# Kernel tuning notes

Measured on AMD Instinct MI355X. Metric: run time of the kernel, lower is better.

The kernel has to match this reference:

```python
import jax, jax.numpy as jnp
import numpy as np

N_STATE = 64
N_LAYERS = 4
D_MODEL = 512
D_OUT = 256
BATCH = 16
SEQLEN = 2048


def setup_inputs() -> dict:
    key = jax.random.key(0)
    ks = jax.random.split(key, 16)
    H, N, nl = D_MODEL, N_STATE, N_LAYERS
    inp = {}
    inp["x"] = jax.random.normal(ks[0], (BATCH, SEQLEN, D_MODEL), dtype=jnp.float32)
    # encoder / decoder dense
    inp["enc_w"] = jax.random.normal(ks[1], (D_MODEL, D_MODEL), jnp.float32) / np.sqrt(D_MODEL)
    inp["enc_b"] = jnp.zeros((D_MODEL,), jnp.float32)
    inp["dec_w"] = jax.random.normal(ks[2], (D_MODEL, D_OUT), jnp.float32) / np.sqrt(D_MODEL)
    inp["dec_b"] = jnp.zeros((D_OUT,), jnp.float32)
    # per-layer LayerNorm
    inp["ln_scale"] = jnp.ones((nl, D_MODEL), jnp.float32)
    inp["ln_bias"] = jnp.zeros((nl, D_MODEL), jnp.float32)
    # per-layer S4 DPLR params (stored as real/imag float pairs)
    inp["lambda_re"] = -0.5 * jnp.ones((nl, H, N), jnp.float32)
    inp["lambda_im"] = jnp.broadcast_to(np.pi * jnp.arange(N, dtype=jnp.float32), (nl, H, N))
    inp["p_re"] = jax.random.normal(ks[3], (nl, H, N), jnp.float32) * 0.5
    inp["p_im"] = jax.random.normal(ks[4], (nl, H, N), jnp.float32) * 0.5
    inp["b_re"] = jax.random.normal(ks[5], (nl, H, N), jnp.float32) * 0.5
    inp["b_im"] = jax.random.normal(ks[6], (nl, H, N), jnp.float32) * 0.5
    inp["c_re"] = jax.random.normal(ks[7], (nl, H, N), jnp.float32) * 0.5
    inp["c_im"] = jax.random.normal(ks[8], (nl, H, N), jnp.float32) * 0.5
    inp["log_step"] = jax.random.uniform(ks[9], (nl, H), jnp.float32, minval=np.log(1e-3), maxval=np.log(1e-1))
    inp["d_param"] = jnp.ones((nl, H), jnp.float32)
    # per-layer output Dense
    inp["out_w"] = jax.random.normal(ks[10], (nl, D_MODEL, D_MODEL), jnp.float32) / np.sqrt(D_MODEL)
    inp["out_b"] = jnp.zeros((nl, D_MODEL), jnp.float32)
    return inp


def _layer_norm(x, scale, bias, eps=1e-6):
    mu = jnp.mean(x, axis=-1, keepdims=True)
    var = jnp.mean(jnp.square(x - mu), axis=-1, keepdims=True)
    return (x - mu) * jax.lax.rsqrt(var + eps) * scale + bias


def _kernel_dplr(Lam, P, B, C, step, L):
    # Lam,P,B,C: [H,N] complex64; step: [H] float32 -> K: [H,L] float32
    theta = (2.0 * np.pi / L) * jnp.arange(L, dtype=jnp.float32)
    Omega = jnp.exp(-1j * theta)                        # [L] roots of unity
    g = (2.0 / step)[:, None] * ((1.0 - Omega) / (1.0 + Omega))[None, :]  # [H,L]
    c = 2.0 / (1.0 + Omega)                             # [L]
    r = 1.0 / (g[:, :, None] - Lam[:, None, :])         # [H,L,N] resolvent (Cauchy)
    Cc, Pc = jnp.conj(C), jnp.conj(P)
    k00 = jnp.einsum("hn,hln->hl", Cc * B, r)
    k01 = jnp.einsum("hn,hln->hl", Cc * P, r)
    k10 = jnp.einsum("hn,hln->hl", Pc * B, r)
    k11 = jnp.einsum("hn,hln->hl", Pc * P, r)
    at_roots = c[None, :] * (k00 - k01 * (1.0 / (1.0 + k11)) * k10)  # [H,L]
    return jnp.fft.ifft(at_roots, n=L, axis=-1).real


def _s4_apply(u, Lam, P, B, C, step, D):
    # u: [Bt,L,H]; causal FFT convolution with kernel K[h,:] per channel
    L = u.shape[1]
    K = _kernel_dplr(Lam, P, B, C, step, L)             # [H,L]
    ud = jnp.fft.rfft(u, n=2 * L, axis=1)               # [Bt,L+1,H]
    Kd = jnp.fft.rfft(K, n=2 * L, axis=-1)              # [H,L+1]
    y = jnp.fft.irfft(ud * Kd.T[None], n=2 * L, axis=1)[:, :L]
    return y + D[None, None, :] * u


def reference(x, enc_w, enc_b, ln_scale, ln_bias, lambda_re, lambda_im,
              p_re, p_im, b_re, b_im, c_re, c_im, log_step, d_param,
              out_w, out_b, dec_w, dec_b):
    h = x @ enc_w + enc_b
    n_layers = ln_scale.shape[0]
    for i in range(n_layers):
        skip = h
        z = _layer_norm(h, ln_scale[i], ln_bias[i])
        Lam = lambda_re[i] + 1j * lambda_im[i]
        P = p_re[i] + 1j * p_im[i]
        B = b_re[i] + 1j * b_im[i]
        C = c_re[i] + 1j * c_im[i]
        z = _s4_apply(z, Lam, P, B, C, jnp.exp(log_step[i]), d_param[i])
        z = jax.nn.gelu(z)
        z = z @ out_w[i] + out_b[i]
        h = skip + z  # dropout=0.0 -> identity
    logits = h @ dec_w + dec_b
    return jax.nn.log_softmax(logits, axis=-1)
```

## Files before the change

kernel.cpp:

```cpp
#include <hip/hip_runtime.h>
#include <hip/hip_bf16.h>

#define NLAY 4
#define DH   512
#define NST  64
#define NB   16
#define SL   2048
#define NDO  256
#define BL   (NB*SL)
#define KDIM 512
#define TWOPI 6.283185307179586476925287

typedef unsigned short u16;
typedef __attribute__((ext_vector_type(8))) short  short8v;
typedef __attribute__((ext_vector_type(8))) unsigned short ushort8v;
typedef __attribute__((ext_vector_type(4))) float  f32x4;
typedef __attribute__((ext_vector_type(2))) unsigned int uint2v;

#define RCPF(x) __builtin_amdgcn_rcpf(x)

__device__ __forceinline__ float bf2f(u16 v){
  union { unsigned u; float f; } x; x.u = ((unsigned)v) << 16; return x.f;
}
__device__ __forceinline__ u16 f2bf(float f){
  union { float f; unsigned u; } x; x.f = f;
  unsigned u = x.u;
  unsigned r = u + 0x7fffu + ((u >> 16) & 1u);
  return (u16)(r >> 16);
}
__device__ __forceinline__ void cmulw(float& xr, float& xi, float wr, float wi){
  float tr = xr*wr - xi*wi;
  xi = fmaf(xr, wi, xi*wr);
  xr = tr;
}
__device__ __forceinline__ float gelu_fast(float v){
  const float c0 = 0.7978845608028654f;
  float u = c0 * fmaf(0.044715f, v*v*v, v);
  return v * RCPF(1.0f + __expf(-2.0f * u));
}
__device__ __forceinline__ void gload16(const void* g, void* l){
  __builtin_amdgcn_global_load_lds(
      (__attribute__((address_space(1))) void*)(g),
      (__attribute__((address_space(3))) void*)(l), 16, 0, 0);
}

__device__ __forceinline__ void twapply(float* re, float* im, float a){
  float ci, cr;
  __sincosf(a, &ci, &cr);
  float wr = cr, wi = ci;
#pragma unroll
  for (int k = 1; k < 16; k++){
    cmulw(re[k], im[k], wr, wi);
    const float nr = wr*cr - wi*ci;
    wi = fmaf(wr, ci, wi*cr);
    wr = nr;
  }
}

template<int SGN>
__device__ __forceinline__ void dft4w(float& r0, float& i0, float& r1, float& i1,
                                      float& r2, float& i2, float& r3, float& i3){
  const float t0r = r0 + r2, t0i = i0 + i2;
  const float t1r = r0 - r2, t1i = i0 - i2;
  const float t2r = r1 + r3, t2i = i1 + i3;
  const float t3r = r1 - r3, t3i = i1 - i3;
  r0 = t0r + t2r; i0 = t0i + t2i;
  r2 = t0r - t2r; i2 = t0i - t2i;
  if (SGN < 0){ r1 = t1r + t3i; i1 = t1i - t3r; r3 = t1r - t3i; i3 = t1i + t3r; }
  else        { r1 = t1r - t3i; i1 = t1i + t3r; r3 = t1r + t3i; i3 = t1i - t3r; }
}

template<int SGN>
__device__ __forceinline__ void dft16(float* re, float* im){
#pragma unroll
  for (int b = 0; b < 4; b++)
    dft4w<SGN>(re[b], im[b], re[4+b], im[4+b], re[8+b], im[8+b], re[12+b], im[12+b]);
  const float C1 = 0.92387953251128675613f, S1_ = 0.38268343236508977172f;
  const float C2 = 0.70710678118654752440f;
  const float sg = (SGN < 0) ? -1.f : 1.f;
  cmulw(re[5],  im[5],   C1,  sg*S1_);
  cmulw(re[9],  im[9],   C2,  sg*C2);
  cmulw(re[13], im[13],  S1_, sg*C1);
  cmulw(re[6],  im[6],   C2,  sg*C2);
  cmulw(re[10], im[10],  0.f, sg*1.f);
  cmulw(re[14], im[14], -C2,  sg*C2);
  cmulw(re[7],  im[7],   S1_, sg*C1);
  cmulw(re[11], im[11], -C2,  sg*C2);
  cmulw(re[15], im[15], -C1,  sg*(-S1_));
#pragma unroll
  for (int c = 0; c < 4; c++)
    dft4w<SGN>(re[4*c], im[4*c], re[4*c+1], im[4*c+1], re[4*c+2], im[4*c+2], re[4*c+3], im[4*c+3]);
  float tr_, ti_;
#define SWP(A,B) tr_=re[A]; re[A]=re[B]; re[B]=tr_; ti_=im[A]; im[A]=im[B]; im[B]=ti_;
  SWP(1,4) SWP(2,8) SWP(3,12) SWP(6,9) SWP(7,13) SWP(11,14)
#undef SWP
}

__device__ __forceinline__ int cxpad(int i){ return i + (i >> 4) + ((i >> 8) << 1); }
#define CXSZ 4384

__device__ __forceinline__ void fwd4096(float* re, float* im, float2* cx, int t){
  dft16<-1>(re, im);
  twapply(re, im, -(float)(TWOPI/4096.0) * (float)t);
#pragma unroll
  for (int k = 0; k < 16; k++) cx[cxpad(t + 256*k)] = make_float2(re[k], im[k]);
  __syncthreads();
  const int k1 = t >> 4, m2 = t & 15;
  const int b2 = k1*256 + m2;
#pragma unroll
  for (int j = 0; j < 16; j++){ float2 v = cx[cxpad(b2 + 16*j)]; re[j] = v.x; im[j] = v.y; }
  dft16<-1>(re, im);
  twapply(re, im, -(float)(TWOPI/256.0) * (float)m2);
#pragma unroll
  for (int k = 0; k < 16; k++) cx[cxpad(b2 + 16*k)] = make_float2(re[k], im[k]);
  __syncthreads();
#pragma unroll
  for (int j = 0; j < 16; j++){ float2 v = cx[cxpad(16*t + j)]; re[j] = v.x; im[j] = v.y; }
  dft16<-1>(re, im);
}

__device__ __forceinline__ void inv4096(float* re, float* im, float2* cx, int t){
  dft16<1>(re, im);
#pragma unroll
  for (int j = 0; j < 16; j++) cx[cxpad(16*t + j)] = make_float2(re[j], im[j]);
  __syncthreads();
  const int k1 = t >> 4, m2 = t & 15;
  const int b2 = k1*256 + m2;
#pragma unroll
  for (int k = 0; k < 16; k++){ float2 v = cx[cxpad(b2 + 16*k)]; re[k] = v.x; im[k] = v.y; }
  twapply(re, im, (float)(TWOPI/256.0) * (float)m2);
  dft16<1>(re, im);
#pragma unroll
  for (int j = 0; j < 16; j++) cx[cxpad(b2 + 16*j)] = make_float2(re[j], im[j]);
  __syncthreads();
#pragma unroll
  for (int k = 0; k < 16; k++){ float2 v = cx[cxpad(t + 256*k)]; re[k] = v.x; im[k] = v.y; }
  twapply(re, im, (float)(TWOPI/4096.0) * (float)t);
  dft16<1>(re, im);
}

__global__ __launch_bounds__(256) void prep_k(
  const float* __restrict__ lam_re, const float* __restrict__ lam_im,
  const float* __restrict__ p_re,  const float* __restrict__ p_im,
  const float* __restrict__ b_re,  const float* __restrict__ b_im,
  const float* __restrict__ c_re,  const float* __restrict__ c_im,
  float4* __restrict__ cwA, float4* __restrict__ cwB, float* __restrict__ cwS)
{
  const int i = blockIdx.x * 256 + threadIdx.x;
  const float lr = lam_re[i], li = lam_im[i];
  const float pr = p_re[i],  pi = p_im[i];
  const float br = b_re[i],  bi = b_im[i];
  const float cr = c_re[i],  ci = c_im[i];
  cwA[i] = make_float4(lr, li, cr*br + ci*bi, cr*bi - ci*br);
  cwB[i] = make_float4(cr*pr + ci*pi, cr*pi - ci*pr, pr*br + pi*bi, pr*bi - pi*br);
  cwS[i] = pr*pr + pi*pi;
}

__global__ __launch_bounds__(256) void cauchy_k(
    const float4* __restrict__ cwA, const float4* __restrict__ cwB,
    const float* __restrict__ cwS, const float* __restrict__ lstep,
    float2* __restrict__ Kd)
{
  const int t = threadIdx.x;
  const int h = blockIdx.y, lay = blockIdx.z;
  const int lb = blockIdx.x * 256 + t;
  const int wb = (lay*DH + h) * NST;
  const float tw0 = 2.0f * expf(-lstep[lay*DH + h]);

  float T0,T1, g0,g1;
  { float sn, cs;
    sincosf((float)(TWOPI/4096.0)*(float)(lb       ), &sn, &cs); T0 = sn*RCPF(cs); g0 = tw0*T0;
    sincosf((float)(TWOPI/4096.0)*(float)(lb + 1024), &sn, &cs); T1 = sn*RCPF(cs); g1 = tw0*T1;
  }

  float k00r0=0,k00i0=0,k01r0=0,k01i0=0,k10r0=0,k10i0=0,k11r0=0,k11i0=0;
  float k00r1=0,k00i1=0,k01r1=0,k01i1=0,k10r1=0,k10i1=0,k11r1=0,k11i1=0;

#pragma unroll 2
  for (int n = 0; n < NST; n++){
    const float4 A  = cwA[wb + n];
    const float4 Bv = cwB[wb + n];
    const float w11 = cwS[wb + n];
    const float nlr = -A.x;
    const float dr2 = A.x * A.x;
#define CSTEP(J) { \
    const float di = g##J - A.y; \
    const float sI = RCPF(fmaf(di, di, dr2)); \
    const float ivr = nlr * sI, ivi = -di * sI; \
    k00r##J = fmaf(A.z,  ivr, fmaf(-A.w,  ivi, k00r##J)); \
    k00i##J = fmaf(A.z,  ivi, fmaf( A.w,  ivr, k00i##J)); \
    k01r##J = fmaf(Bv.x, ivr, fmaf(-Bv.y, ivi, k01r##J)); \
    k01i##J = fmaf(Bv.x, ivi, fmaf( Bv.y, ivr, k01i##J)); \
    k10r##J = fmaf(Bv.z, ivr, fmaf(-Bv.w, ivi, k10r##J)); \
    k10i##J = fmaf(Bv.z, ivi, fmaf( Bv.w, ivr, k10i##J)); \
    k11r##J = fmaf(w11,  ivr, k11r##J); \
    k11i##J = fmaf(w11,  ivi, k11i##J); }
    CSTEP(0) CSTEP(1)
#undef CSTEP
  }

  float2* kp = Kd + (size_t)(lay*DH + h) * 4096;
#define COUT(J, LOFF) { \
    const float d1r = 1.f + k11r##J, d1i = k11i##J; \
    const float idn = RCPF(fmaf(d1r, d1r, d1i*d1i)); \
    const float wr = k01r##J*k10r##J - k01i##J*k10i##J; \
    const float wi = k01r##J*k10i##J + k01i##J*k10r##J; \
    const float vr = fmaf(wr, d1r,  wi*d1i) * idn; \
    const float vi = fmaf(wi, d1r, -wr*d1i) * idn; \
    const float sr = k00r##J - vr, si = k00i##J - vi; \
    kp[lb + LOFF] = make_float2(fmaf(-T##J, si, sr), fmaf(T##J, sr, si)); }
  COUT(0, 0) COUT(1, 1024)
#undef COUT
}

__global__ __launch_bounds__(256) void kdfft_k(float2* __restrict__ Kd){
  __shared__ float  ar[SL], ai[SL];
  __shared__ float2 cx[CXSZ];
  const int t = threadIdx.x;
  const size_t base = (size_t)blockIdx.x * 4096;
#pragma unroll
  for (int q = 0; q < 8; q++){
    const int l = t + 256*q;
    float2 v = Kd[base + l];
    const int brv = __brev((unsigned)l) >> 21;
    ar[brv] = v.x; ai[brv] = v.y;
  }
  __syncthreads();

  for (int s = 0; s < 11; s++){
    const int half = 1 << s;
    const float fac = (float)(TWOPI) / (float)(2 << s);
#pragma unroll
    for (int q = 0; q < 4; q++){
      const int v = t + 256*q;
      const int pos = v & (half - 1);
      const int i0 = ((v >> s) << (s+1)) + pos;
      const int i1 = i0 + half;
      const float ang = fac * (float)pos;
      const float wc = __cosf(ang), ws = __sinf(ang);
      const float xr = ar[i1], xi = ai[i1];
      const float tr = wc*xr - ws*xi, ti = fmaf(wc, xi, ws*xr);
      const float ur_ = ar[i0], ui_ = ai[i0];
      ar[i0] = ur_ + tr; ai[i0] = ui_ + ti;
      ar[i1] = ur_ - tr; ai[i1] = ui_ - ti;
    }
    __syncthreads();
  }

  float re[16], im[16];
#pragma unroll
  for (int j = 0; j < 16; j++){
    re[j] = (j < 8) ? ar[t + 256*j] * (1.0f/2048.f) : 0.f;
    im[j] = 0.f;
  }
  fwd4096(re, im, cx, t);
  float2* kp = Kd + base + 16*t;
#pragma unroll
  for (int k = 0; k < 16; k += 2)
    *(float4*)(kp + k) = make_float4(re[k], im[k], re[k+1], im[k+1]);
}

__global__ __launch_bounds__(256) void wconv_all_k(
    const float* __restrict__ enc_w, const float* __restrict__ out_w,
    const float* __restrict__ dec_w, u16* __restrict__ Wt)
{
  const int z = blockIdx.z;
  const float* src; u16* dst; int N;
  if (z == 0){ src = enc_w; dst = Wt; N = DH; }
  else if (z <= 4){ src = out_w + (size_t)(z-1)*KDIM*DH; dst = Wt + (size_t)z*262144; N = DH; }
  else { if (blockIdx.y >= 4) return; src = dec_w; dst = Wt + (size_t)5*262144; N = NDO; }
  __shared__ u16 tile[64][72];
  const int k0 = blockIdx.x * 64, n0 = blockIdx.y * 64;
  const int r = threadIdx.x >> 2, c4 = (threadIdx.x & 3) * 16;
  const float* s = src + (size_t)(k0 + r) * N + n0 + c4;
  float4 f0 = *(const float4*)s, f1 = *(const float4*)(s+4);
  float4 f2 = *(const float4*)(s+8), f3 = *(const float4*)(s+12);
  tile[c4+0][r]=f2bf(f0.x); tile[c4+1][r]=f2bf(f0.y); tile[c4+2][r]=f2bf(f0.z); tile[c4+3][r]=f2bf(f0.w);
  tile[c4+4][r]=f2bf(f1.x); tile[c4+5][r]=f2bf(f1.y); tile[c4+6][r]=f2bf(f1.z); tile[c4+7][r]=f2bf(f1.w);
  tile[c4+8][r]=f2bf(f2.x); tile[c4+9][r]=f2bf(f2.y); tile[c4+10][r]=f2bf(f2.z); tile[c4+11][r]=f2bf(f2.w);
  tile[c4+12][r]=f2bf(f3.x); tile[c4+13][r]=f2bf(f3.y); tile[c4+14][r]=f2bf(f3.z); tile[c4+15][r]=f2bf(f3.w);
  __syncthreads();
  u16* d = dst + (size_t)(n0 + r) * KDIM + k0 + c4;
  *(ushort8v*)d       = *(const ushort8v*)&tile[r][c4];
  *(ushort8v*)(d + 8) = *(const ushort8v*)&tile[r][c4 + 8];
}

#define LTILE 32
__device__ __forceinline__ int lnswz(int h){ return ((h >> 1) + (h >> 6)) & 3; }

__global__ __launch_bounds__(256) void lnt_k(const u16* __restrict__ hsrc,
    const float* __restrict__ gam, const float* __restrict__ bet,
    u16* __restrict__ zT){
  __shared__ u16 tile[DH][LTILE];
  __shared__ float smu[LTILE], srs[LTILE];
  const int t = threadIdx.x;
  const int b = blockIdx.y, l0 = blockIdx.x * LTILE;
  const int r = t >> 3, hb = (t & 7) * 64;
  const u16* p = hsrc + ((size_t)b * SL + l0 + r) * DH + hb;
  float s = 0.f, sq = 0.f;
#pragma unroll
  for (int j8 = 0; j8 < 8; j8++){
    ushort8v w = *(const ushort8v*)(p + j8*8);
    const int h0 = hb + j8*8;
#pragma unroll
    for (int d = 0; d < 8; d++){
      const float f = bf2f((u16)w[d]);
      s += f; sq = fmaf(f, f, sq);
      tile[h0+d][r ^ (lnswz(h0+d) << 3)] = (u16)w[d];
    }
  }
  s  += __shfl_xor(s, 1);  sq += __shfl_xor(sq, 1);
  s  += __shfl_xor(s, 2);  sq += __shfl_xor(sq, 2);
  s  += __shfl_xor(s, 4);  sq += __shfl_xor(sq, 4);
  if ((t & 7) == 0){
    const float mu = s * (1.0f/DH);
    smu[r] = mu;
    srs[r] = rsqrtf(sq * (1.0f/DH) - mu*mu + 1e-6f);
  }
  __syncthreads();

#pragma unroll
  for (int hh = 0; hh < 2; hh++){
    const int h = t + hh*256;
    const float g = gam[h], be = bet[h];
    const int sw = lnswz(h);
    u16* dst = zT + ((size_t)b * DH + h) * SL + l0;
#pragma unroll
    for (int og = 0; og < 4; og++){
      const int lg = og ^ sw;
      ushort8v v = *(const ushort8v*)&tile[h][og*8];
      const float4 m0 = *(const float4*)&smu[lg*8];
      const float4 m1 = *(const float4*)&smu[lg*8 + 4];
      const float4 r0 = *(const float4*)&srs[lg*8];
      const float4 r1 = *(const float4*)&srs[lg*8 + 4];
      ushort8v o;
      o[0] = f2bf(fmaf(bf2f((u16)v[0]) - m0.x, r0.x*g, be));
      o[1] = f2bf(fmaf(bf2f((u16)v[1]) - m0.y, r0.y*g, be));
      o[2] = f2bf(fmaf(bf2f((u16)v[2]) - m0.z, r0.z*g, be));
      o[3] = f2bf(fmaf(bf2f((u16)v[3]) - m0.w, r0.w*g, be));
      o[4] = f2bf(fmaf(bf2f((u16)v[4]) - m1.x, r1.x*g, be));
      o[5] = f2bf(fmaf(bf2f((u16)v[5]) - m1.y, r1.y*g, be));
      o[6] = f2bf(fmaf(bf2f((u16)v[6]) - m1.z, r1.z*g, be));
      o[7] = f2bf(fmaf(bf2f((u16)v[7]) - m1.w, r1.w*g, be));
      *(ushort8v*)(dst + lg*8) = o;
    }
  }
}

__global__ __launch_bounds__(256) void s4conv_k(
    const u16* __restrict__ zT, const float2* __restrict__ Kd,
    const float* __restrict__ dpar, u16* __restrict__ yT)
{
  __shared__ float2 cx[CXSZ];
  const int t = threadIdx.x;
  const int wg = blockIdx.x;
  const int h = wg & 511, bp = wg >> 9;
  const u16* r1 = zT + ((size_t)(2*bp) * DH + h) * SL;
  const u16* r2 = r1 + (size_t)DH * SL;
  float ur1[8], ur2[8];
  float re[16], im[16];
#pragma unroll
  for (int j = 0; j < 8; j++){
    ur1[j] = bf2f(r1[t + 256*j]);
    ur2[j] = bf2f(r2[t + 256*j]);
    re[j] = ur1[j]; im[j] = ur2[j];
  }
#pragma unroll
  for (int j = 8; j < 16; j++){ re[j] = 0.f; im[j] = 0.f; }

  fwd4096(re, im, cx, t);

  const float2* kp = Kd + (size_t)h * 4096 + 16*t;
#pragma unroll
  for (int k = 0; k < 16; k += 2){
    float4 w2 = *(const float4*)(kp + k);
    cmulw(re[k],   im[k],   w2.x, w2.y);
    cmulw(re[k+1], im[k+1], w2.z, w2.w);
  }

  inv4096(re, im, cx, t);

  const float Dv = dpar[h];
  u16* y1 = yT + ((size_t)(2*bp) * DH + h) * SL;
  u16* y2 = y1 + (size_t)DH * SL;
#pragma unroll
  for (int j = 0; j < 8; j++){
    float v1 = fmaf(re[j], (1.0f/4096.f), Dv * ur1[j]);
    float v2 = fmaf(im[j], (1.0f/4096.f), Dv * ur2[j]);
    y1[t + 256*j] = f2bf(gelu_fast(v1));
    y2[t + 256*j] = f2bf(gelu_fast(v2));
  }
}

__global__ __launch_bounds__(256) void gemm_at_k(
    const u16* __restrict__ A, const u16* __restrict__ Wt,
    const float* __restrict__ bias,
    const u16* __restrict__ resid, u16* __restrict__ Cout,
    int Mb, int N)
{
  __shared__ u16 As[4096];
  __shared__ u16 Bs[4096];
  const int t = threadIdx.x;
  const int n0 = blockIdx.x * 128, m0 = blockIdx.y * 128, bb = blockIdx.z;
  const int lane = t & 63, wv = t >> 6;
  const int wm = (wv >> 1) * 64, wn = (wv & 1) * 64;
  const int wbase = t & 192;
  f32x4 acc[4][4];
#pragma unroll
  for (int mi = 0; mi < 4; mi++)
#pragma unroll
    for (int ni = 0; ni < 4; ni++) acc[mi][ni] = {0.f, 0.f, 0.f, 0.f};

  int kA[2], mA[2];
#pragma unroll
  for (int i = 0; i < 2; i++){
    const int G = i*256 + t;
    const int s = G >> 3, r8 = G & 7;
    const int q = s & 7;
    const int kb = ((q & 3) << 1) | (q >> 2);
    kA[i] = kb*4 + (r8 >> 1);
    mA[i] = (s >> 3)*16 + (r8 & 1)*8;
  }
  const size_t Abase = (size_t)bb * DH * (size_t)Mb;
  const unsigned lds_as =
      (unsigned)(unsigned long long)(__attribute__((address_space(3))) u16*)As;

  for (int k0 = 0; k0 < KDIM; k0 += 32){
    __syncthreads();
#pragma unroll
    for (int i = 0; i < 2; i++)
      gload16(A + Abase + (size_t)(k0 + kA[i]) * Mb + m0 + mA[i],
              As + (size_t)(i*256 + wbase) * 8);
#pragma unroll
    for (int i = 0; i < 2; i++){
      const int G = i*256 + t;
      const int r = G >> 2;
      const int g = ((G & 3) ^ r ^ (r >> 2)) & 3;
      gload16(Wt + (size_t)(n0 + r) * KDIM + k0 + g*8,
              Bs + (size_t)(i*256 + wbase) * 8);
    }
    __syncthreads();

    uint2v ra[4], rb[4];
#pragma unroll
    for (int mi = 0; mi < 4; mi++){
      const unsigned b = lds_as + (unsigned)(((wm >> 4) + mi) * 1024 + lane * 8);
      asm volatile("ds_read_b64_tr_b16 %0, %1" : "=v"(ra[mi]) : "v"(b));
      asm volatile("ds_read_b64_tr_b16 %0, %1 offset:512" : "=v"(rb[mi]) : "v"(b));
    }
    asm volatile("s_waitcnt lgkmcnt(0)" ::: "memory");
    __builtin_amdgcn_sched_barrier(0);

    short8v af[4], bf[4];
#pragma unroll
    for (int mi = 0; mi < 4; mi++){
      union { uint2v u2[2]; short8v s8; } cvt;
      cvt.u2[0] = ra[mi]; cvt.u2[1] = rb[mi];
      af[mi] = cvt.s8;
    }
    const int fr = lane & 15, g4 = lane >> 4;
#pragma unroll
    for (int ni = 0; ni < 4; ni++){
      const int r = wn + ni*16 + fr;
      bf[ni] = *(const short8v*)&Bs[(size_t)((r<<2) | ((g4 ^ r ^ (r>>2)) & 3)) * 8];
    }
#pragma unroll
    for (int mi = 0; mi < 4; mi++)
#pragma unroll
      for (int ni = 0; ni < 4; ni++)
        acc[mi][ni] = __builtin_amdgcn_mfma_f32_16x16x32_bf16(af[mi], bf[ni], acc[mi][ni], 0, 0, 0);
  }

  const int fr = lane & 15;
  const int rq = (lane >> 4) * 4;
#pragma unroll
  for (int mi = 0; mi < 4; mi++){
#pragma unroll
    for (int ni = 0; ni < 4; ni++){
      const int gn = n0 + wn + ni*16 + fr;
      const float bs = bias[gn];
#pragma unroll
      for (int q = 0; q < 4; q++){
        const int gm = m0 + wm + mi*16 + rq + q;
        const size_t idx = ((size_t)bb * Mb + gm) * N + gn;
        Cout[idx] = f2bf(acc[mi][ni][q] + bs + bf2f(resid[idx]));
      }
    }
  }
}

template<int AMODE, bool OUTBF>
__global__ __launch_bounds__(256) void gemm_k(
    const void* __restrict__ Aptr, const u16* __restrict__ Wt,
    const float* __restrict__ bias, void* __restrict__ Coutv,
    int Mb, int N)
{
  __shared__ u16 As[4096];
  __shared__ u16 Bs[4096];
  const int t = threadIdx.x;
  const int n0 = blockIdx.x * 128, m0 = blockIdx.y * 128;
  const int lane = t & 63, wv = t >> 6;
  const int wm = (wv >> 1) * 64, wn = (wv & 1) * 64;
  const int wbase = t & 192;
  f32x4 acc[4][4];
#pragma unroll
  for (int mi = 0; mi < 4; mi++)
#pragma unroll
    for (int ni = 0; ni < 4; ni++) acc[mi][ni] = {0.f, 0.f, 0.f, 0.f};

  const u16*  Ab = (const u16*)Aptr;
  const float* Af = (const float*)Aptr;

  for (int k0 = 0; k0 < KDIM; k0 += 32){
    __syncthreads();
    if (AMODE == 0){
#pragma unroll
      for (int i = 0; i < 2; i++){
        const int G = i*256 + t;
        const int r = G >> 2;
        const int g = ((G & 3) ^ r ^ (r >> 2)) & 3;
        gload16(Ab + (size_t)(m0 + r) * KDIM + k0 + g*8,
                As + (size_t)(i*256 + wbase) * 8);
      }
    } else {
      const int r = t >> 1, kh = (t & 1) << 4;
      const float* sf = Af + (size_t)(m0 + r) * KDIM + k0 + kh;
      float4 f0 = *(const float4*)sf,     f1 = *(const float4*)(sf + 4);
      float4 f2 = *(const float4*)(sf+8), f3 = *(const float4*)(sf + 12);
      ushort8v v0, v1;
      v0[0]=f2bf(f0.x); v0[1]=f2bf(f0.y); v0[2]=f2bf(f0.z); v0[3]=f2bf(f0.w);
      v0[4]=f2bf(f1.x); v0[5]=f2bf(f1.y); v0[6]=f2bf(f1.z); v0[7]=f2bf(f1.w);
      v1[0]=f2bf(f2.x); v1[1]=f2bf(f2.y); v1[2]=f2bf(f2.z); v1[3]=f2bf(f2.w);
      v1[4]=f2bf(f3.x); v1[5]=f2bf(f3.y); v1[6]=f2bf(f3.z); v1[7]=f2bf(f3.w);
      const int key = (r ^ (r >> 2)) & 3;
      *(ushort8v*)&As[(size_t)((r<<2) | ((kh>>3) ^ key))*8]       = v0;
      *(ushort8v*)&As[(size_t)((r<<2) | (((kh>>3)+1) ^ key))*8]   = v1;
    }
#pragma unroll
    for (int i = 0; i < 2; i++){
      const int G = i*256 + t;
      const int r = G >> 2;
      const int g = ((G & 3) ^ r ^ (r >> 2)) & 3;
      gload16(Wt + (size_t)(n0 + r) * KDIM + k0 + g*8,
              Bs + (size_t)(i*256 + wbase) * 8);
    }
    __syncthreads();

    const int fr = lane & 15, g4 = lane >> 4;
    short8v af[4], bf[4];
#pragma unroll
    for (int mi = 0; mi < 4; mi++){
      const int r = wm + mi*16 + fr;
      af[mi] = *(const short8v*)&As[(size_t)((r<<2) | ((g4 ^ r ^ (r>>2)) & 3)) * 8];
    }
#pragma unroll
    for (int ni = 0; ni < 4; ni++){
      const int r = wn + ni*16 + fr;
      bf[ni] = *(const short8v*)&Bs[(size_t)((r<<2) | ((g4 ^ r ^ (r>>2)) & 3)) * 8];
    }
#pragma unroll
    for (int mi = 0; mi < 4; mi++)
#pragma unroll
      for (int ni = 0; ni < 4; ni++)
        acc[mi][ni] = __builtin_amdgcn_mfma_f32_16x16x32_bf16(af[mi], bf[ni], acc[mi][ni], 0, 0, 0);
  }

  const int fr = lane & 15;
  const int rq = (lane >> 4) * 4;
#pragma unroll
  for (int mi = 0; mi < 4; mi++){
#pragma unroll
    for (int ni = 0; ni < 4; ni++){
      const int gn = n0 + wn + ni*16 + fr;
      const float bs = bias[gn];
#pragma unroll
      for (int q = 0; q < 4; q++){
        const int gm = m0 + wm + mi*16 + rq + q;
        const size_t idx = (size_t)gm * N + gn;
        float v = acc[mi][ni][q] + bs;
        if (OUTBF) ((u16*)Coutv)[idx] = f2bf(v);
        else       ((float*)Coutv)[idx] = v;
      }
    }
  }
}

__global__ __launch_bounds__(256) void lsm_k(float* __restrict__ o){
  const int row = blockIdx.x * 4 + (threadIdx.x >> 6);
  const int lane = threadIdx.x & 63;
  float* p = o + (size_t)row * NDO + lane * 4;
  float4 v = *(const float4*)p;
  float mx = fmaxf(fmaxf(v.x, v.y), fmaxf(v.z, v.w));
#pragma unroll
  for (int q = 32; q; q >>= 1) mx = fmaxf(mx, __shfl_xor(mx, q));
  float e = __expf(v.x - mx) + __expf(v.y - mx) + __expf(v.z - mx) + __expf(v.w - mx);
#pragma unroll
  for (int q = 32; q; q >>= 1) e += __shfl_xor(e, q);
  const float lse = mx + __logf(e);
  v.x -= lse; v.y -= lse; v.z -= lse; v.w -= lse;
  *(float4*)p = v;
}

extern "C" void kernel_launch(void* const* d_in, const int* in_sizes, int n_in,
                              void* d_out, int out_size, void* d_ws, size_t ws_size,
                              hipStream_t stream)
{
  (void)in_sizes; (void)n_in; (void)out_size; (void)ws_size;
  const float* x      = (const float*)d_in[0];
  const float* enc_w  = (const float*)d_in[1];
  const float* enc_b  = (const float*)d_in[2];
  const float* dec_w  = (const float*)d_in[3];
  const float* dec_b  = (const float*)d_in[4];
  const float* ln_s   = (const float*)d_in[5];
  const float* ln_b   = (const float*)d_in[6];
  const float* lam_re = (const float*)d_in[7];
  const float* lam_im = (const float*)d_in[8];
  const float* p_re   = (const float*)d_in[9];
  const float* p_im   = (const float*)d_in[10];
  const float* b_re   = (const float*)d_in[11];
  const float* b_im   = (const float*)d_in[12];
  const float* c_re   = (const float*)d_in[13];
  const float* c_im   = (const float*)d_in[14];
  const float* lstep  = (const float*)d_in[15];
  const float* d_par  = (const float*)d_in[16];
  const float* out_w  = (const float*)d_in[17];
  const float* out_b  = (const float*)d_in[18];

  char* ws = (char*)d_ws;
  u16*    hbuf = (u16*)(ws);
  u16*    zT   = (u16*)  (ws + (size_t)67108864 + 33554432);
  u16*    yT   = (u16*)  (ws + (size_t)67108864 + 2*33554432);
  float2* Kd   = (float2*)(ws + (size_t)67108864 + 3*33554432);
  u16*    Wt   = (u16*)  (ws + (size_t)67108864 + 3*33554432 + 67108864);
  u16*    WtOut = Wt + 262144;
  u16*    WtDec = Wt + 262144*5;
  float*  outp = (float*)d_out;

  float4* cwA = (float4*)d_out;
  float4* cwB = cwA + 131072;
  float*  cwS = (float*)(cwB + 131072);

  prep_k<<<dim3(NLAY*DH*NST/256), 256, 0, stream>>>(lam_re, lam_im, p_re, p_im,
                                                    b_re, b_im, c_re, c_im, cwA, cwB, cwS);
  wconv_all_k<<<dim3(8, 8, 6), 256, 0, stream>>>(enc_w, out_w, dec_w, Wt);
  cauchy_k<<<dim3(4, DH, NLAY), 256, 0, stream>>>(cwA, cwB, cwS, lstep, Kd);
  kdfft_k<<<dim3(NLAY*DH), 256, 0, stream>>>(Kd);
  gemm_k<2,true><<<dim3(DH/128, BL/128, 1), 256, 0, stream>>>(
      x, Wt, enc_b, hbuf, BL, DH);
  for (int i = 0; i < NLAY; i++){
    lnt_k<<<dim3(SL/LTILE, NB), 256, 0, stream>>>(hbuf, ln_s + i*DH, ln_b + i*DH, zT);
    s4conv_k<<<dim3((NB/2)*DH), 256, 0, stream>>>(
        zT, Kd + (size_t)i*DH*4096, d_par + i*DH, yT);
    gemm_at_k<<<dim3(DH/128, SL/128, NB), 256, 0, stream>>>(
        yT, WtOut + (size_t)i*262144, out_b + i*DH, hbuf, hbuf, SL, DH);
  }
  gemm_k<0,false><<<dim3(NDO/128, BL/128, 1), 256, 0, stream>>>(
      hbuf, WtDec, dec_b, outp, BL, NDO);
  lsm_k<<<dim3(BL/4), 256, 0, stream>>>(outp);
}
```

Measured before the change: 707.2 us.

## Fuse log-softmax into decoder GEMM and exploit zero-padded half in forward FFT

The decoder GEMM now computes a full 128x256 row tile per block, so log-softmax runs in the epilogue with cross-lane shuffles. This removes the separate lsm_k launch and the extra read and write of the fp32 logits. The first radix-16 stage of the 4096-point forward FFT now assumes the upper half of the inputs is zero (the zero-padding for n=2L), which skips half of its butterfly work. The fused GEMM holds 32 accumulator vectors per thread, which raises register pressure, halves the block count and may lower occupancy.

```diff
diff --git a/kernel.cpp b/kernel.cpp
--- a/kernel.cpp
+++ b/kernel.cpp
@@ -71,10 +71,7 @@
 }
 
 template<int SGN>
-__device__ __forceinline__ void dft16(float* re, float* im){
-#pragma unroll
-  for (int b = 0; b < 4; b++)
-    dft4w<SGN>(re[b], im[b], re[4+b], im[4+b], re[8+b], im[8+b], re[12+b], im[12+b]);
+__device__ __forceinline__ void dft16tail(float* re, float* im){
   const float C1 = 0.92387953251128675613f, S1_ = 0.38268343236508977172f;
   const float C2 = 0.70710678118654752440f;
   const float sg = (SGN < 0) ? -1.f : 1.f;
@@ -96,11 +93,31 @@
 #undef SWP
 }
 
+template<int SGN>
+__device__ __forceinline__ void dft16(float* re, float* im){
+#pragma unroll
+  for (int b = 0; b < 4; b++)
+    dft4w<SGN>(re[b], im[b], re[4+b], im[4+b], re[8+b], im[8+b], re[12+b], im[12+b]);
+  dft16tail<SGN>(re, im);
+}
+
+__device__ __forceinline__ void dft16fh(float* re, float* im){
+#pragma unroll
+  for (int b = 0; b < 4; b++){
+    const float r0 = re[b], i0 = im[b], r1 = re[4+b], i1 = im[4+b];
+    re[b]    = r0 + r1; im[b]    = i0 + i1;
+    re[4+b]  = r0 + i1; im[4+b]  = i0 - r1;
+    re[8+b]  = r0 - r1; im[8+b]  = i0 - i1;
+    re[12+b] = r0 - i1; im[12+b] = i0 + r1;
+  }
+  dft16tail<-1>(re, im);
+}
+
 __device__ __forceinline__ int cxpad(int i){ return i + (i >> 4) + ((i >> 8) << 1); }
 #define CXSZ 4384
 
 __device__ __forceinline__ void fwd4096(float* re, float* im, float2* cx, int t){
-  dft16<-1>(re, im);
+  dft16fh(re, im);
   twapply(re, im, -(float)(TWOPI/4096.0) * (float)t);
 #pragma unroll
   for (int k = 0; k < 16; k++) cx[cxpad(t + 256*k)] = make_float2(re[k], im[k]);
@@ -489,10 +506,9 @@
   }
 }
 
-template<int AMODE, bool OUTBF>
-__global__ __launch_bounds__(256) void gemm_k(
-    const void* __restrict__ Aptr, const u16* __restrict__ Wt,
-    const float* __restrict__ bias, void* __restrict__ Coutv,
+__global__ __launch_bounds__(256) void gemm_enc_k(
+    const float* __restrict__ Af, const u16* __restrict__ Wt,
+    const float* __restrict__ bias, u16* __restrict__ Cout,
     int Mb, int N)
 {
   __shared__ u16 As[4096];
@@ -508,21 +524,9 @@
 #pragma unroll
     for (int ni = 0; ni < 4; ni++) acc[mi][ni] = {0.f, 0.f, 0.f, 0.f};
 
-  const u16*  Ab = (const u16*)Aptr;
-  const float* Af = (const float*)Aptr;
-
   for (int k0 = 0; k0 < KDIM; k0 += 32){
     __syncthreads();
-    if (AMODE == 0){
-#pragma unroll
-      for (int i = 0; i < 2; i++){
-        const int G = i*256 + t;
-        const int r = G >> 2;
-        const int g = ((G & 3) ^ r ^ (r >> 2)) & 3;
-        gload16(Ab + (size_t)(m0 + r) * KDIM + k0 + g*8,
-                As + (size_t)(i*256 + wbase) * 8);
-      }
-    } else {
+    {
       const int r = t >> 1, kh = (t & 1) << 4;
       const float* sf = Af + (size_t)(m0 + r) * KDIM + k0 + kh;
       float4 f0 = *(const float4*)sf,     f1 = *(const float4*)(sf + 4);
@@ -576,29 +580,102 @@
 #pragma unroll
       for (int q = 0; q < 4; q++){
         const int gm = m0 + wm + mi*16 + rq + q;
-        const size_t idx = (size_t)gm * N + gn;
-        float v = acc[mi][ni][q] + bs;
-        if (OUTBF) ((u16*)Coutv)[idx] = f2bf(v);
-        else       ((float*)Coutv)[idx] = v;
+        Cout[(size_t)gm * N + gn] = f2bf(acc[mi][ni][q] + bs);
       }
     }
   }
 }
 
-__global__ __launch_bounds__(256) void lsm_k(float* __restrict__ o){
-  const int row = blockIdx.x * 4 + (threadIdx.x >> 6);
-  const int lane = threadIdx.x & 63;
-  float* p = o + (size_t)row * NDO + lane * 4;
-  float4 v = *(const float4*)p;
-  float mx = fmaxf(fmaxf(v.x, v.y), fmaxf(v.z, v.w));
-#pragma unroll
-  for (int q = 32; q; q >>= 1) mx = fmaxf(mx, __shfl_xor(mx, q));
-  float e = __expf(v.x - mx) + __expf(v.y - mx) + __expf(v.z - mx) + __expf(v.w - mx);
-#pragma unroll
-  for (int q = 32; q; q >>= 1) e += __shfl_xor(e, q);
-  const float lse = mx + __logf(e);
-  v.x -= lse; v.y -= lse; v.z -= lse; v.w -= lse;
-  *(float4*)p = v;
+__global__ __launch_bounds__(256) void gemm_dec_k(
+    const u16* __restrict__ A, const u16* __restrict__ Wt,
+    const float* __restrict__ bias, float* __restrict__ Out)
+{
+  __shared__ u16 As[4096];
+  __shared__ u16 Bs[8192];
+  const int t = threadIdx.x;
+  const int m0 = blockIdx.x * 128;
+  const int lane = t & 63, wv = t >> 6;
+  const int wm = wv * 32;
+  const int wbase = t & 192;
+  f32x4 acc[2][16];
+#pragma unroll
+  for (int mi = 0; mi < 2; mi++)
+#pragma unroll
+    for (int ni = 0; ni < 16; ni++) acc[mi][ni] = {0.f, 0.f, 0.f, 0.f};
+
+  for (int k0 = 0; k0 < KDIM; k0 += 32){
+    __syncthreads();
+#pragma unroll
+    for (int i = 0; i < 2; i++){
+      const int G = i*256 + t;
+      const int r = G >> 2;
+      const int g = ((G & 3) ^ r ^ (r >> 2)) & 3;
+      gload16(A + (size_t)(m0 + r) * KDIM + k0 + g*8,
+              As + (size_t)(i*256 + wbase) * 8);
+    }
+#pragma unroll
+    for (int i = 0; i < 4; i++){
+      const int G = i*256 + t;
+      const int r = G >> 2;
+      const int g = ((G & 3) ^ r ^ (r >> 2)) & 3;
+      gload16(Wt + (size_t)r * KDIM + k0 + g*8,
+              Bs + (size_t)(i*256 + wbase) * 8);
+    }
+    __syncthreads();
+
+    const int fr = lane & 15, g4 = lane >> 4;
+    short8v af[2], bf[16];
+#pragma unroll
+    for (int mi = 0; mi < 2; mi++){
+      const int r = wm + mi*16 + fr;
+      af[mi] = *(const short8v*)&As[(size_t)((r<<2) | ((g4 ^ r ^ (r>>2)) & 3)) * 8];
+    }
+#pragma unroll
+    for (int ni = 0; ni < 16; ni++){
+      const int r = ni*16 + fr;
+      bf[ni] = *(const short8v*)&Bs[(size_t)((r<<2) | ((g4 ^ r ^ (r>>2)) & 3)) * 8];
+    }
+#pragma unroll
+    for (int mi = 0; mi < 2; mi++)
+#pragma unroll
+      for (int ni = 0; ni < 16; ni++)
+        acc[mi][ni] = __builtin_amdgcn_mfma_f32_16x16x32_bf16(af[mi], bf[ni], acc[mi][ni], 0, 0, 0);
+  }
+
+  const int fr = lane & 15, g4 = lane >> 4;
+  float bssv[16];
+#pragma unroll
+  for (int ni = 0; ni < 16; ni++) bssv[ni] = bias[ni*16 + fr];
+
+#pragma unroll
+  for (int mi = 0; mi < 2; mi++){
+#pragma unroll
+    for (int q = 0; q < 4; q++){
+      float v[16];
+      float mx = -3.4e38f;
+#pragma unroll
+      for (int ni = 0; ni < 16; ni++){
+        v[ni] = acc[mi][ni][q] + bssv[ni];
+        mx = fmaxf(mx, v[ni]);
+      }
+      mx = fmaxf(mx, __shfl_xor(mx, 1));
+      mx = fmaxf(mx, __shfl_xor(mx, 2));
+      mx = fmaxf(mx, __shfl_xor(mx, 4));
+      mx = fmaxf(mx, __shfl_xor(mx, 8));
+      float e = 0.f;
+#pragma unroll
+      for (int ni = 0; ni < 16; ni++) e += __expf(v[ni] - mx);
+      e += __shfl_xor(e, 1);
+      e += __shfl_xor(e, 2);
+      e += __shfl_xor(e, 4);
+      e += __shfl_xor(e, 8);
+      const float lse = mx + __logf(e);
+      const int gm = m0 + wm + mi*16 + g4*4 + q;
+      float* po = Out + (size_t)gm * NDO + fr;
+#pragma unroll
+      for (int ni = 0; ni < 16; ni++) po[ni*16] = v[ni] - lse;
+    }
+  }
 }
 
 extern "C" void kernel_launch(void* const* d_in, const int* in_sizes, int n_in,
@@ -645,7 +722,7 @@
   wconv_all_k<<<dim3(8, 8, 6), 256, 0, stream>>>(enc_w, out_w, dec_w, Wt);
   cauchy_k<<<dim3(4, DH, NLAY), 256, 0, stream>>>(cwA, cwB, cwS, lstep, Kd);
   kdfft_k<<<dim3(NLAY*DH), 256, 0, stream>>>(Kd);
-  gemm_k<2,true><<<dim3(DH/128, BL/128, 1), 256, 0, stream>>>(
+  gemm_enc_k<<<dim3(DH/128, BL/128, 1), 256, 0, stream>>>(
       x, Wt, enc_b, hbuf, BL, DH);
   for (int i = 0; i < NLAY; i++){
     lnt_k<<<dim3(SL/LTILE, NB), 256, 0, stream>>>(hbuf, ln_s + i*DH, ln_b + i*DH, zT);
@@ -654,7 +731,5 @@
     gemm_at_k<<<dim3(DH/128, SL/128, NB), 256, 0, stream>>>(
         yT, WtOut + (size_t)i*262144, out_b + i*DH, hbuf, hbuf, SL, DH);
   }
-  gemm_k<0,false><<<dim3(NDO/128, BL/128, 1), 256, 0, stream>>>(
-      hbuf, WtDec, dec_b, outp, BL, NDO);
-  lsm_k<<<dim3(BL/4), 256, 0, stream>>>(outp);
-}
+  gemm_dec_k<<<dim3(BL/128), 256, 0, stream>>>(hbuf, WtDec, dec_b, outp);
+}
```

New measurement: 700.6 us. Within noise of the previous version (-0.9%).
